# Optimization experiments

Measured on AMD Instinct MI355X. Metric: run time of the kernel, lower is better.

## Reference

```python
import jax, jax.numpy as jnp
import numpy as np

B, H, S, D = 2, 16, 2048, 128


def alibi_slopes(n_heads: int) -> jnp.ndarray:
    # Standard ALiBi geometric slopes: 2^(-8*(h+1)/n_heads)
    h = jnp.arange(n_heads, dtype=jnp.float32)
    return jnp.exp2(-8.0 * (h + 1.0) / n_heads)


def setup_inputs() -> dict:
    key = jax.random.key(0)
    kq, kk, kv = jax.random.split(key, 3)
    q = jax.random.normal(kq, (B, H, S, D), dtype=jnp.float32)
    k = jax.random.normal(kk, (B, H, S, D), dtype=jnp.float32)
    v = jax.random.normal(kv, (B, H, S, D), dtype=jnp.float32)
    return {"q": q, "k": k, "v": v}


def reference(q, k, v):
    # FlexAttention forward: causal block mask + ALiBi score_mod, default scale 1/sqrt(D)
    d = q.shape[-1]
    scale = 1.0 / jnp.sqrt(jnp.asarray(d, dtype=q.dtype))
    slopes = alibi_slopes(q.shape[1]).astype(q.dtype)  # [H]

    scores = jnp.einsum("bhqd,bhkd->bhqk", q, k) * scale  # [B,H,S,S]
    q_idx = jnp.arange(q.shape[2])[:, None]   # [S,1]
    kv_idx = jnp.arange(k.shape[2])[None, :]  # [1,S]
    # score_mod: score + slopes[h] * (kv - q)  (bias <= 0 in causal region)
    bias = slopes[None, :, None, None] * (kv_idx - q_idx).astype(q.dtype)[None, None]
    scores = scores + bias
    causal = q_idx >= kv_idx  # [S,S]
    neg_inf = jnp.asarray(-jnp.inf, dtype=scores.dtype)
    scores = jnp.where(causal[None, None], scores, neg_inf)
    probs = jax.nn.softmax(scores, axis=-1)
    return jnp.einsum("bhqk,bhkd->bhqd", probs, v)
```

## Files before the change

kernel.cpp:

```cpp
#include <hip/hip_runtime.h>
#include <hip/hip_bf16.h>

#define BB 2
#define HH 16
#define SS 2048
#define DD 128

constexpr int BM = 64;
constexpr int BN = 64;
constexpr int NW = 4;
constexpr int PSTR = BN + 8;
constexpr size_t SD = (size_t)SS * DD;
constexpr size_t KV_ELEMS = (size_t)BB * HH * SS * DD;

typedef __bf16 bf16_t;
typedef __attribute__((ext_vector_type(8))) __bf16 bf16x8;
typedef __attribute__((ext_vector_type(4))) __bf16 bf16x4;
typedef __attribute__((ext_vector_type(4))) float floatx4;

__device__ __forceinline__ void dma16(const void* g, void* l) {
    __builtin_amdgcn_global_load_lds(
        (const __attribute__((address_space(1))) unsigned int*)g,
        (__attribute__((address_space(3))) unsigned int*)l,
        16, 0, 0);
}

__global__ __launch_bounds__(256)
void prep_kv(const float* __restrict__ kp, const float* __restrict__ vp,
             bf16_t* __restrict__ kbf, bf16_t* __restrict__ vtbf)
{
    __shared__ __align__(16) bf16_t VT[64][140];

    const int tid  = threadIdx.x;
    const int kv0  = blockIdx.x * BN;
    const size_t bh = blockIdx.y;

    const float* kb = kp + bh * SD;
    const float* vb = vp + bh * SD;
    bf16_t* ko = kbf  + bh * SD;
    bf16_t* vo = vtbf + bh * (size_t)DD * SS;

    #pragma unroll
    for (int i = 0; i < 8; ++i) {
        int idx4 = tid + i * 256;
        int row  = idx4 >> 5;
        int c4   = idx4 & 31;
        float4 val = *reinterpret_cast<const float4*>(vb + (size_t)(kv0 + row) * DD + c4 * 4);
        bf16x4 o;
        o[0] = (bf16_t)val.x; o[1] = (bf16_t)val.y; o[2] = (bf16_t)val.z; o[3] = (bf16_t)val.w;
        *reinterpret_cast<bf16x4*>(&VT[row][c4 * 4]) = o;
    }

    #pragma unroll
    for (int i = 0; i < 8; ++i) {
        int idx4 = tid + i * 256;
        int row  = idx4 >> 5;
        int c4   = idx4 & 31;
        float4 val = *reinterpret_cast<const float4*>(kb + (size_t)(kv0 + row) * DD + c4 * 4);
        bf16x4 o;
        o[0] = (bf16_t)val.x; o[1] = (bf16_t)val.y; o[2] = (bf16_t)val.z; o[3] = (bf16_t)val.w;
        *reinterpret_cast<bf16x4*>(ko + (size_t)(kv0 + row) * DD + c4 * 4) = o;
    }

    __syncthreads();

    const int kv8 = (tid & 7) * 8;
    const int dg  = tid >> 3;
    #pragma unroll
    for (int i = 0; i < 4; ++i) {
        int d = dg + i * 32;
        bf16x8 w;
        #pragma unroll
        for (int j = 0; j < 8; ++j)
            w[j] = VT[kv8 + j][d];
        *reinterpret_cast<bf16x8*>(vo + (size_t)d * SS + kv0 + kv8) = w;
    }
}

__global__ __launch_bounds__(256, 2)
void flexattn_fwd_bf16(const float* __restrict__ qp, const bf16_t* __restrict__ kbf,
                       const bf16_t* __restrict__ vtbf, float* __restrict__ op)
{
    __shared__ __align__(16) bf16_t KV[2][2][8192];
    __shared__ __align__(16) bf16_t Ps[NW][16][PSTR];

    const int tid  = threadIdx.x;
    const int wave = tid >> 6;
    const int lane = tid & 63;
    const int n16  = lane & 15;
    const int quad = lane >> 4;

    const int lid  = blockIdx.y * gridDim.x + blockIdx.x;
    const int xcd  = lid & 7;
    const int slot = lid >> 3;
    const int nl   = xcd * ((SS / BM) * BB * HH / 8) + slot;
    const int bh   = nl >> 5;
    const int qt   = 31 - (nl & 31);
    const int h    = bh & (HH - 1);
    const int q0   = qt * BM;

    const float LOG2E  = 1.4426950408889634f;
    const float sscale = 0.08838834764831845f * LOG2E;
    const float slope  = __builtin_amdgcn_exp2f(-8.0f * (float)(h + 1) / (float)HH);
    const float bscale = slope * LOG2E;

    const float*  qb = qp   + (size_t)bh * SD;
    const bf16_t* kb = kbf  + (size_t)bh * SD;
    const bf16_t* vt = vtbf + (size_t)bh * (size_t)DD * SS;
    float*        ob = op   + (size_t)bh * SD;

    const int q = q0 + wave * 16 + n16;

    int koff[4], voff[4];
    #pragma unroll
    for (int i = 0; i < 4; ++i) {
        int c   = wave * 256 + i * 64 + lane;
        int kv  = c >> 4;
        int col = (c & 15) ^ (kv & 15);
        koff[i] = kv * 256 + col * 16;
        int d  = c >> 3;
        int jp = c & 7;
        int j  = jp ^ (d & 7) ^ (((d >> 3) & 1) << 2);
        voff[i] = (d * SS + j * 8) * 2;
    }

    auto dma_tile = [&](int kt, int b) {
        const char* kg = (const char*)kb + (size_t)kt * (BN * DD * 2);
        const char* vg = (const char*)vt + (size_t)kt * (BN * 2);
        char* kl = (char*)&KV[b][0][0];
        char* vl = (char*)&KV[b][1][0];
        #pragma unroll
        for (int i = 0; i < 4; ++i) {
            int base = (wave * 256 + i * 64) * 16;
            dma16(kg + koff[i], kl + base);
            dma16(vg + voff[i], vl + base);
        }
    };

    bf16x8 qf[4];
    #pragma unroll
    for (int c = 0; c < 4; ++c) {
        const float* qs = qb + (size_t)q * DD + c * 32 + quad * 8;
        float4 a = *reinterpret_cast<const float4*>(qs);
        float4 b = *reinterpret_cast<const float4*>(qs + 4);
        qf[c][0] = (bf16_t)a.x; qf[c][1] = (bf16_t)a.y;
        qf[c][2] = (bf16_t)a.z; qf[c][3] = (bf16_t)a.w;
        qf[c][4] = (bf16_t)b.x; qf[c][5] = (bf16_t)b.y;
        qf[c][6] = (bf16_t)b.z; qf[c][7] = (bf16_t)b.w;
    }

    dma_tile(0, 0);

    floatx4 o[8];
    #pragma unroll
    for (int t = 0; t < 8; ++t) o[t] = (floatx4){0.f, 0.f, 0.f, 0.f};
    float l_i = 0.f;

    const int bias_base = quad * 4 - q;

    int kfo[4];
    #pragma unroll
    for (int c = 0; c < 4; ++c)
        kfo[c] = n16 * 256 + (((c * 4 + quad) ^ n16) * 16);
    const int vkey = (n16 & 7) ^ (((n16 >> 3) & 1) << 2);
    int vfo[2];
    #pragma unroll
    for (int c = 0; c < 2; ++c)
        vfo[c] = n16 * 128 + (((c * 4 + quad) ^ vkey) * 16);

    __syncthreads();

    for (int kt = 0; kt <= qt; ++kt) {
        const int kv0 = kt * BN;
        const int b   = kt & 1;
        if (kt < qt) dma_tile(kt + 1, b ^ 1);

        const char* kl = (const char*)&KV[b][0][0];
        const char* vl = (const char*)&KV[b][1][0];

        floatx4 sc[4];
        __builtin_amdgcn_s_setprio(1);
        #pragma unroll
        for (int nt = 0; nt < 4; ++nt) {
            floatx4 acc = (floatx4){0.f, 0.f, 0.f, 0.f};
            #pragma unroll
            for (int c = 0; c < 4; ++c) {
                bf16x8 kf = *reinterpret_cast<const bf16x8*>(kl + nt * 4096 + kfo[c]);
                acc = __builtin_amdgcn_mfma_f32_16x16x32_bf16(kf, qf[c], acc, 0, 0, 0);
            }
            sc[nt] = acc;
        }
        __builtin_amdgcn_s_setprio(0);

        const bool diag = (kt == qt);
        float rs = 0.f;
        #pragma unroll
        for (int nt = 0; nt < 4; ++nt) {
            #pragma unroll
            for (int r = 0; r < 4; ++r) {
                int delta = kv0 + nt * 16 + r + bias_base;
                float sval = sc[nt][r] * sscale + (bscale * (float)delta - 8.0f);
                if (diag && delta > 0) sval = -3.0e38f;
                float p = __builtin_amdgcn_exp2f(sval);
                sc[nt][r] = p;
                rs += p;
            }
        }
        l_i += rs;

        bf16x8 p0, p1;
        #pragma unroll
        for (int r = 0; r < 4; ++r) {
            p0[r]     = (bf16_t)sc[0][r];
            p0[r + 4] = (bf16_t)sc[1][r];
            p1[r]     = (bf16_t)sc[2][r];
            p1[r + 4] = (bf16_t)sc[3][r];
        }
        *reinterpret_cast<bf16x8*>(&Ps[wave][n16][quad * 16])     = p0;
        *reinterpret_cast<bf16x8*>(&Ps[wave][n16][quad * 16 + 8]) = p1;

        bf16x8 pf[2];
        #pragma unroll
        for (int c = 0; c < 2; ++c) {
            #pragma unroll
            for (int j4 = 0; j4 < 2; ++j4) {
                int s0 = (((2 * quad + j4) & 3) * 16) + ((2 * c + (quad >> 1)) * 4);
                bf16x4 ph = *reinterpret_cast<const bf16x4*>(&Ps[wave][n16][s0]);
                pf[c][j4 * 4 + 0] = ph[0];
                pf[c][j4 * 4 + 1] = ph[1];
                pf[c][j4 * 4 + 2] = ph[2];
                pf[c][j4 * 4 + 3] = ph[3];
            }
        }

        __builtin_amdgcn_s_setprio(1);
        #pragma unroll
        for (int t = 0; t < 8; ++t) {
            floatx4 acc = o[t];
            #pragma unroll
            for (int c = 0; c < 2; ++c) {
                bf16x8 vf = *reinterpret_cast<const bf16x8*>(vl + t * 2048 + vfo[c]);
                acc = __builtin_amdgcn_mfma_f32_16x16x32_bf16(vf, pf[c], acc, 0, 0, 0);
            }
            o[t] = acc;
        }
        __builtin_amdgcn_s_setprio(0);

        __syncthreads();
    }

    float lt = l_i;
    lt += __shfl_xor(lt, 16);
    lt += __shfl_xor(lt, 32);
    const float inv = 1.0f / lt;
    const size_t rowoff = (size_t)q * DD;
    #pragma unroll
    for (int t = 0; t < 8; ++t) {
        float4 w;
        w.x = o[t][0] * inv; w.y = o[t][1] * inv;
        w.z = o[t][2] * inv; w.w = o[t][3] * inv;
        *reinterpret_cast<float4*>(ob + rowoff + t * 16 + quad * 4) = w;
    }
}

extern "C" void kernel_launch(void* const* d_in, const int* in_sizes, int n_in,
                              void* d_out, int out_size, void* d_ws, size_t ws_size,
                              hipStream_t stream) {
    const float* q = (const float*)d_in[0];
    const float* k = (const float*)d_in[1];
    const float* v = (const float*)d_in[2];
    float* out = (float*)d_out;

    bf16_t* kbf  = (bf16_t*)d_ws;
    bf16_t* vtbf = kbf + KV_ELEMS;
    prep_kv<<<dim3(SS / BN, BB * HH), 256, 0, stream>>>(k, v, kbf, vtbf);
    flexattn_fwd_bf16<<<dim3(SS / BM, BB * HH), 256, 0, stream>>>(q, kbf, vtbf, out);
}
```

Before: 206.9 us.

## Switch attention to 32x32x16 MFMA with split-KV waves and register-only P transfer

Replaces the 16x16x32 MFMA tiling with 32x32x16 MFMAs. The four waves are now arranged as 2 query halves by 2 key halves, and the partial O and row sums are combined through LDS at the end. The P tile no longer round-trips through a shared-memory buffer; it is packed with v_cvt_pk_bf16 and rearranged across lanes with v_permlane32_swap. A wave skips its masked diagonal subtile entirely. This trades LDS traffic and per-MFMA overhead for a final cross-wave reduction and larger accumulator register use, which could lower occupancy.

Measured after the change: 187.2 us. 9.5% less time.

```diff
diff --git a/kernel.cpp b/kernel.cpp
--- a/kernel.cpp
+++ b/kernel.cpp
@@ -9,20 +9,32 @@
 constexpr int BM = 64;
 constexpr int BN = 64;
 constexpr int NW = 4;
-constexpr int PSTR = BN + 8;
 constexpr size_t SD = (size_t)SS * DD;
 constexpr size_t KV_ELEMS = (size_t)BB * HH * SS * DD;
 
 typedef __bf16 bf16_t;
+typedef unsigned int u32;
 typedef __attribute__((ext_vector_type(8))) __bf16 bf16x8;
 typedef __attribute__((ext_vector_type(4))) __bf16 bf16x4;
 typedef __attribute__((ext_vector_type(4))) float floatx4;
+typedef __attribute__((ext_vector_type(16))) float floatx16;
+typedef __attribute__((ext_vector_type(4))) unsigned int u32x4;
 
 __device__ __forceinline__ void dma16(const void* g, void* l) {
     __builtin_amdgcn_global_load_lds(
         (const __attribute__((address_space(1))) unsigned int*)g,
         (__attribute__((address_space(3))) unsigned int*)l,
         16, 0, 0);
+}
+
+__device__ __forceinline__ u32 cvt_pk_bf16(float lo, float hi) {
+    u32 r;
+    asm("v_cvt_pk_bf16_f32 %0, %1, %2" : "=v"(r) : "v"(lo), "v"(hi));
+    return r;
+}
+
+__device__ __forceinline__ void plane32_swap(u32& a, u32& b) {
+    asm("v_permlane32_swap_b32 %0, %1" : "+v"(a), "+v"(b));
 }
 
 __global__ __launch_bounds__(256)
@@ -82,13 +94,14 @@
                        const bf16_t* __restrict__ vtbf, float* __restrict__ op)
 {
     __shared__ __align__(16) bf16_t KV[2][2][8192];
-    __shared__ __align__(16) bf16_t Ps[NW][16][PSTR];
-
-    const int tid  = threadIdx.x;
-    const int wave = tid >> 6;
-    const int lane = tid & 63;
-    const int n16  = lane & 15;
-    const int quad = lane >> 4;
+
+    const int tid   = threadIdx.x;
+    const int wave  = tid >> 6;
+    const int lane  = tid & 63;
+    const int l31   = lane & 31;
+    const int lhalf = lane >> 5;
+    const int qh    = wave >> 1;
+    const int kh    = wave & 1;
 
     const int lid  = blockIdx.y * gridDim.x + blockIdx.x;
     const int xcd  = lid & 7;
@@ -109,7 +122,7 @@
     const bf16_t* vt = vtbf + (size_t)bh * (size_t)DD * SS;
     float*        ob = op   + (size_t)bh * SD;
 
-    const int q = q0 + wave * 16 + n16;
+    const int q = q0 + qh * 32 + l31;
 
     int koff[4], voff[4];
     #pragma unroll
@@ -137,36 +150,46 @@
         }
     };
 
-    bf16x8 qf[4];
-    #pragma unroll
-    for (int c = 0; c < 4; ++c) {
-        const float* qs = qb + (size_t)q * DD + c * 32 + quad * 8;
+    bf16x8 qf[8];
+    #pragma unroll
+    for (int dc = 0; dc < 8; ++dc) {
+        const float* qs = qb + (size_t)q * DD + dc * 16 + lhalf * 8;
         float4 a = *reinterpret_cast<const float4*>(qs);
         float4 b = *reinterpret_cast<const float4*>(qs + 4);
-        qf[c][0] = (bf16_t)a.x; qf[c][1] = (bf16_t)a.y;
-        qf[c][2] = (bf16_t)a.z; qf[c][3] = (bf16_t)a.w;
-        qf[c][4] = (bf16_t)b.x; qf[c][5] = (bf16_t)b.y;
-        qf[c][6] = (bf16_t)b.z; qf[c][7] = (bf16_t)b.w;
+        qf[dc][0] = (bf16_t)a.x; qf[dc][1] = (bf16_t)a.y;
+        qf[dc][2] = (bf16_t)a.z; qf[dc][3] = (bf16_t)a.w;
+        qf[dc][4] = (bf16_t)b.x; qf[dc][5] = (bf16_t)b.y;
+        qf[dc][6] = (bf16_t)b.z; qf[dc][7] = (bf16_t)b.w;
     }
 
     dma_tile(0, 0);
 
-    floatx4 o[8];
-    #pragma unroll
-    for (int t = 0; t < 8; ++t) o[t] = (floatx4){0.f, 0.f, 0.f, 0.f};
+    floatx16 zero16;
+    #pragma unroll
+    for (int i = 0; i < 16; ++i) zero16[i] = 0.f;
+
+    floatx16 o[4];
+    #pragma unroll
+    for (int t = 0; t < 4; ++t) o[t] = zero16;
     float l_i = 0.f;
 
-    const int bias_base = quad * 4 - q;
-
-    int kfo[4];
-    #pragma unroll
-    for (int c = 0; c < 4; ++c)
-        kfo[c] = n16 * 256 + (((c * 4 + quad) ^ n16) * 16);
-    const int vkey = (n16 & 7) ^ (((n16 >> 3) & 1) << 2);
-    int vfo[2];
-    #pragma unroll
-    for (int c = 0; c < 2; ++c)
-        vfo[c] = n16 * 128 + (((c * 4 + quad) ^ vkey) * 16);
+    const int kbase0 = kh * 32 - q;
+
+    int kfo[8];
+    const int krow = kh * 32 + l31;
+    #pragma unroll
+    for (int dc = 0; dc < 8; ++dc)
+        kfo[dc] = krow * 256 + (((dc * 2 + lhalf) ^ (krow & 15)) * 16);
+
+    int vfo[4][2];
+    #pragma unroll
+    for (int t = 0; t < 4; ++t) {
+        int row = t * 32 + l31;
+        int key = (row & 7) ^ (((row >> 3) & 1) << 2);
+        #pragma unroll
+        for (int m = 0; m < 2; ++m)
+            vfo[t][m] = row * 128 + (((kh * 4 + m * 2 + lhalf) ^ key) * 16);
+    }
 
     __syncthreads();
 
@@ -177,89 +200,91 @@
 
         const char* kl = (const char*)&KV[b][0][0];
         const char* vl = (const char*)&KV[b][1][0];
-
-        floatx4 sc[4];
-        __builtin_amdgcn_s_setprio(1);
-        #pragma unroll
-        for (int nt = 0; nt < 4; ++nt) {
-            floatx4 acc = (floatx4){0.f, 0.f, 0.f, 0.f};
-            #pragma unroll
-            for (int c = 0; c < 4; ++c) {
-                bf16x8 kf = *reinterpret_cast<const bf16x8*>(kl + nt * 4096 + kfo[c]);
-                acc = __builtin_amdgcn_mfma_f32_16x16x32_bf16(kf, qf[c], acc, 0, 0, 0);
-            }
-            sc[nt] = acc;
-        }
-        __builtin_amdgcn_s_setprio(0);
-
         const bool diag = (kt == qt);
-        float rs = 0.f;
-        #pragma unroll
-        for (int nt = 0; nt < 4; ++nt) {
-            #pragma unroll
-            for (int r = 0; r < 4; ++r) {
-                int delta = kv0 + nt * 16 + r + bias_base;
-                float sval = sc[nt][r] * sscale + (bscale * (float)delta - 8.0f);
+
+        if (!(diag && qh == 0 && kh == 1)) {
+            floatx16 acc = zero16;
+            __builtin_amdgcn_s_setprio(1);
+            #pragma unroll
+            for (int dc = 0; dc < 8; ++dc) {
+                bf16x8 kf = *reinterpret_cast<const bf16x8*>(kl + kfo[dc]);
+                acc = __builtin_amdgcn_mfma_f32_32x32x16_bf16(kf, qf[dc], acc, 0, 0, 0);
+            }
+            __builtin_amdgcn_s_setprio(0);
+
+            float pv[16];
+            float rs = 0.f;
+            #pragma unroll
+            for (int reg = 0; reg < 16; ++reg) {
+                int row   = (reg & 3) + 8 * (reg >> 2) + 4 * lhalf;
+                int delta = kv0 + kbase0 + row;
+                float sval = acc[reg] * sscale + (bscale * (float)delta - 8.0f);
                 if (diag && delta > 0) sval = -3.0e38f;
                 float p = __builtin_amdgcn_exp2f(sval);
-                sc[nt][r] = p;
+                pv[reg] = p;
                 rs += p;
             }
+            l_i += rs;
+
+            u32 pk[8];
+            #pragma unroll
+            for (int i = 0; i < 8; ++i)
+                pk[i] = cvt_pk_bf16(pv[2 * i], pv[2 * i + 1]);
+            plane32_swap(pk[0], pk[2]);
+            plane32_swap(pk[1], pk[3]);
+            plane32_swap(pk[4], pk[6]);
+            plane32_swap(pk[5], pk[7]);
+            u32x4 pw0 = {pk[0], pk[1], pk[2], pk[3]};
+            u32x4 pw1 = {pk[4], pk[5], pk[6], pk[7]};
+            bf16x8 pfrag0 = __builtin_bit_cast(bf16x8, pw0);
+            bf16x8 pfrag1 = __builtin_bit_cast(bf16x8, pw1);
+
+            __builtin_amdgcn_s_setprio(1);
+            #pragma unroll
+            for (int t = 0; t < 4; ++t) {
+                bf16x8 vf0 = *reinterpret_cast<const bf16x8*>(vl + vfo[t][0]);
+                o[t] = __builtin_amdgcn_mfma_f32_32x32x16_bf16(vf0, pfrag0, o[t], 0, 0, 0);
+                bf16x8 vf1 = *reinterpret_cast<const bf16x8*>(vl + vfo[t][1]);
+                o[t] = __builtin_amdgcn_mfma_f32_32x32x16_bf16(vf1, pfrag1, o[t], 0, 0, 0);
+            }
+            __builtin_amdgcn_s_setprio(0);
         }
-        l_i += rs;
-
-        bf16x8 p0, p1;
-        #pragma unroll
-        for (int r = 0; r < 4; ++r) {
-            p0[r]     = (bf16_t)sc[0][r];
-            p0[r + 4] = (bf16_t)sc[1][r];
-            p1[r]     = (bf16_t)sc[2][r];
-            p1[r + 4] = (bf16_t)sc[3][r];
+
+        __syncthreads();
+    }
+
+    float lq = l_i + __shfl_xor(l_i, 32);
+
+    float* OX = reinterpret_cast<float*>(&KV[0][0][0]);
+    float* LX = reinterpret_cast<float*>(&KV[1][0][0]);
+
+    if (kh == 1) {
+        #pragma unroll
+        for (int t = 0; t < 4; ++t) {
+            #pragma unroll
+            for (int reg = 0; reg < 16; ++reg) {
+                int d = t * 32 + (reg & 3) + 8 * (reg >> 2) + 4 * lhalf;
+                OX[d * 64 + qh * 32 + l31] = o[t][reg];
+            }
         }
-        *reinterpret_cast<bf16x8*>(&Ps[wave][n16][quad * 16])     = p0;
-        *reinterpret_cast<bf16x8*>(&Ps[wave][n16][quad * 16 + 8]) = p1;
-
-        bf16x8 pf[2];
-        #pragma unroll
-        for (int c = 0; c < 2; ++c) {
-            #pragma unroll
-            for (int j4 = 0; j4 < 2; ++j4) {
-                int s0 = (((2 * quad + j4) & 3) * 16) + ((2 * c + (quad >> 1)) * 4);
-                bf16x4 ph = *reinterpret_cast<const bf16x4*>(&Ps[wave][n16][s0]);
-                pf[c][j4 * 4 + 0] = ph[0];
-                pf[c][j4 * 4 + 1] = ph[1];
-                pf[c][j4 * 4 + 2] = ph[2];
-                pf[c][j4 * 4 + 3] = ph[3];
+        if (lane < 32) LX[qh * 32 + l31] = lq;
+    }
+    __syncthreads();
+    if (kh == 0) {
+        const float linv = 1.0f / (lq + LX[qh * 32 + l31]);
+        #pragma unroll
+        for (int t = 0; t < 4; ++t) {
+            #pragma unroll
+            for (int r4 = 0; r4 < 4; ++r4) {
+                int dbase = t * 32 + 8 * r4 + 4 * lhalf;
+                float4 w;
+                w.x = (o[t][r4 * 4 + 0] + OX[(dbase + 0) * 64 + qh * 32 + l31]) * linv;
+                w.y = (o[t][r4 * 4 + 1] + OX[(dbase + 1) * 64 + qh * 32 + l31]) * linv;
+                w.z = (o[t][r4 * 4 + 2] + OX[(dbase + 2) * 64 + qh * 32 + l31]) * linv;
+                w.w = (o[t][r4 * 4 + 3] + OX[(dbase + 3) * 64 + qh * 32 + l31]) * linv;
+                *reinterpret_cast<float4*>(ob + (size_t)q * DD + dbase) = w;
             }
         }
-
-        __builtin_amdgcn_s_setprio(1);
-        #pragma unroll
-        for (int t = 0; t < 8; ++t) {
-            floatx4 acc = o[t];
-            #pragma unroll
-            for (int c = 0; c < 2; ++c) {
-                bf16x8 vf = *reinterpret_cast<const bf16x8*>(vl + t * 2048 + vfo[c]);
-                acc = __builtin_amdgcn_mfma_f32_16x16x32_bf16(vf, pf[c], acc, 0, 0, 0);
-            }
-            o[t] = acc;
-        }
-        __builtin_amdgcn_s_setprio(0);
-
-        __syncthreads();
-    }
-
-    float lt = l_i;
-    lt += __shfl_xor(lt, 16);
-    lt += __shfl_xor(lt, 32);
-    const float inv = 1.0f / lt;
-    const size_t rowoff = (size_t)q * DD;
-    #pragma unroll
-    for (int t = 0; t < 8; ++t) {
-        float4 w;
-        w.x = o[t][0] * inv; w.y = o[t][1] * inv;
-        w.z = o[t][2] * inv; w.w = o[t][3] * inv;
-        *reinterpret_cast<float4*>(ob + rowoff + t * 16 + quad * 4) = w;
     }
 }
 
```
